# Optimization experiments

Hardware: AMD Instinct MI355X
Metric: run time of the kernel (lower is better)

The kernel has to match this reference:

```python
import jax, jax.numpy as jnp
import numpy as np

A = 9
H = 384
W = 384
MIN_SIZE = 2.0
NMS_THRESH = 0.7
PRE_NMS = 6000
POST_NMS = 300


def _make_anchors():
    # anchors.generate_anchors((H, W), box_sizes): per-cell (x1, y1, w, h) boxes in
    # feature-map coordinates, one box per (anchor, y, x).
    sizes = []
    for s in (4.0, 8.0, 16.0):
        for r in (0.5, 1.0, 2.0):
            sizes.append((s * np.sqrt(r), s / np.sqrt(r)))
    ys, xs = np.meshgrid(np.arange(H, dtype=np.float32), np.arange(W, dtype=np.float32), indexing='ij')
    cx, cy = xs + 0.5, ys + 0.5
    anch = np.stack([
        np.stack([cx - w / 2, cy - h / 2, np.full_like(cx, w), np.full_like(cx, h)], axis=-1)
        for (w, h) in sizes
    ], axis=0)  # [A, H, W, 4]
    return jnp.asarray(anch, jnp.float32)


def setup_inputs() -> dict:
    key = jax.random.key(0)
    k1, k2 = jax.random.split(key)
    scores = jax.random.uniform(k1, (1, A, H, W), dtype=jnp.float32)
    bbox_deltas = jax.random.normal(k2, (1, 4 * A, H, W), dtype=jnp.float32)
    return {
        'scores': scores,
        'bbox_deltas': bbox_deltas,
        'anchor_boxes': _make_anchors(),
        'image_metadata': jnp.zeros((1, 3), jnp.float32),
    }


def _clip_boxes(boxes, length, width):
    # clip_boxes_batch: clamp everything to >=0, convert (x,y,w,h)->(x1,y1,x2,y2),
    # clip to feature-map bounds, convert back.
    b = jnp.maximum(boxes, 0.0)
    x1, y1, w, h = b[..., 0], b[..., 1], b[..., 2], b[..., 3]
    x2 = x1 + w - 1.0
    y2 = y1 + h - 1.0
    x1 = jnp.minimum(x1, length - 1.0)
    y1 = jnp.minimum(y1, width - 1.0)
    x2 = jnp.minimum(x2, length - 1.0)
    y2 = jnp.minimum(y2, width - 1.0)
    return jnp.stack([x1, y1, x2 - x1 + 1.0, y2 - y1 + 1.0], axis=-1)


def _nms(boxes, valid):
    # Faithful port of the source's sequential NMS: repeatedly pick the remaining
    # box with the largest y2, suppress boxes whose intersection / own-area >= thresh.
    x1, y1, w, h = boxes[:, 0], boxes[:, 1], boxes[:, 2], boxes[:, 3]
    x2 = x1 + w - 1.0
    y2 = y1 + h - 1.0
    areas = w * h
    NEG = jnp.float32(-1e30)

    def cond(st):
        v, keep, cnt = st
        return (cnt < POST_NMS) & jnp.any(v)

    def body(st):
        v, keep, cnt = st
        ind = jnp.argmax(jnp.where(v, y2, NEG))
        xx1 = jnp.maximum(x1, x1[ind])
        yy1 = jnp.maximum(y1, y1[ind])
        xx2 = jnp.minimum(x2, x2[ind])
        yy2 = jnp.minimum(y2, y2[ind])
        inter = jnp.maximum(xx2 - xx1 + 1.0, 0.0) * jnp.maximum(yy2 - yy1 + 1.0, 0.0)
        ratio = inter / areas  # intersection over each candidate's own area (as in source)
        nv = v & (ratio < NMS_THRESH)
        nv = nv.at[ind].set(False)
        return nv, keep.at[cnt].set(ind.astype(jnp.int32)), cnt + 1

    keep0 = jnp.full((POST_NMS,), -1, jnp.int32)
    _, keep, cnt = jax.lax.while_loop(cond, body, (valid, keep0, jnp.int32(0)))
    return keep, cnt


def reference(scores, bbox_deltas, anchor_boxes, image_metadata):
    B = 1
    _, _, Hh, Ww = scores.shape
    # two contiguous .view()s compose to a single reshape
    deltas = bbox_deltas.reshape(B, A, Hh, Ww, 4)
    boxes = anchor_boxes[None] + deltas               # [1, A, H, W, 4]
    clipped = _clip_boxes(boxes, float(Hh), float(Ww))
    keep = (clipped[..., 2] >= MIN_SIZE) & (clipped[..., 3] >= MIN_SIZE)

    N = A * Hh * Ww
    boxes_f = clipped.reshape(N, 4)
    scores_f = scores.reshape(N)
    masked = jnp.where(keep.reshape(N), scores_f, jnp.float32(-jnp.inf))

    # descending score sort, PRE_NMS_TOP_N truncation
    order = jnp.argsort(-masked)[:PRE_NMS]
    props = boxes_f[order]                            # [PRE_NMS, 4]
    sc = masked[order]
    valid = jnp.isfinite(sc)

    keep_idx, cnt = _nms(props, valid)
    sel = props[jnp.maximum(keep_idx, 0)]             # [POST_NMS, 4]
    slot_valid = jnp.arange(POST_NMS) < cnt
    out = jnp.where(slot_valid[:, None], sel, 0.0)[None]  # [1, POST_NMS, 4]
    return out
```

## Files before the change

kernel.cpp:

```cpp
#include <hip/hip_runtime.h>
#include <stdint.h>

#define NN 1327104
#define NQ 331776
#define NB 1296
#define PRE_NMS_ 6000
#define POST_NMS_ 300
#define LB_CAP 16384
#define NPAD 6144
#define NWORD 96
#define KB 24
#define MATB 192
#define NREP 8


static __device__ __forceinline__ uint32_t score_key(float s) {
  uint32_t b = __float_as_uint(s);
  uint32_t u = b ^ (((int32_t)b < 0) ? 0xFFFFFFFFu : 0x80000000u);
  return ~u;
}

static __device__ __forceinline__ uint32_t f2s(float v) {
  uint32_t b = __float_as_uint(v);
  return b ^ (((int32_t)b < 0) ? 0xFFFFFFFFu : 0x80000000u);
}

static __device__ __forceinline__ void compute_box(float4 an, float4 de,
    float& x1, float& y1, float& wc, float& hc, bool& keep) {
  float bx = fmaxf(an.x + de.x, 0.0f);
  float by = fmaxf(an.y + de.y, 0.0f);
  float bw = fmaxf(an.z + de.z, 0.0f);
  float bh = fmaxf(an.w + de.w, 0.0f);
  float x2 = bx + bw - 1.0f;
  float y2 = by + bh - 1.0f;
  x1 = fminf(bx, 383.0f);
  y1 = fminf(by, 383.0f);
  x2 = fminf(x2, 383.0f);
  y2 = fminf(y2, 383.0f);
  wc = x2 - x1 + 1.0f;
  hc = y2 - y1 + 1.0f;
  keep = (wc >= 2.0f) && (hc >= 2.0f);
}

static __device__ __forceinline__ uint32_t kb18_of(float s) {
  return (uint32_t)(s * 262144.0f);
}

static __device__ __forceinline__ uint32_t wscan(uint32_t v, int l) {
  #pragma unroll
  for (int off = 1; off < 64; off <<= 1) {
    uint32_t u = __shfl_up(v, off);
    if (l >= off) v += u;
  }
  return v;
}

static __device__ __forceinline__ void pick1_f(const uint32_t* __restrict__ h1r,
                                               uint32_t& selR8, uint32_t& base1) {
  int l = threadIdx.x & 63;
  uint32_t a0 = 0, a1 = 0, a2 = 0, a3 = 0, a4 = 0;
  #pragma unroll
  for (int r = 0; r < NREP; ++r) {
    const uint32_t* h1 = h1r + r * 320;
    a0 += h1[l*5]; a1 += h1[l*5+1]; a2 += h1[l*5+2]; a3 += h1[l*5+3]; a4 += h1[l*5+4];
  }
  uint32_t c0 = a0, c1 = c0+a1, c2 = c1+a2, c3 = c2+a3, c4 = c3+a4;
  uint32_t inc = wscan(c4, l);
  uint32_t excl = inc - c4;
  bool hit = (excl < PRE_NMS_) && (inc >= PRE_NMS_);
  unsigned long long hb = __ballot(hit);
  int hl = __ffsll(hb) - 1;
  uint32_t k, cb;
  if      (excl + c0 >= PRE_NMS_) { k = 0; cb = 0;  }
  else if (excl + c1 >= PRE_NMS_) { k = 1; cb = c0; }
  else if (excl + c2 >= PRE_NMS_) { k = 2; cb = c1; }
  else if (excl + c3 >= PRE_NMS_) { k = 3; cb = c2; }
  else                            { k = 4; cb = c3; }
  selR8 = __shfl(l*5u + k, hl);
  base1 = __shfl(excl + cb, hl);
}

static __device__ __forceinline__ void pickT_lds(const uint32_t* __restrict__ h2,
                                                 uint32_t T,
                                                 uint32_t& sel10, uint32_t& base) {
  int l = threadIdx.x & 63;
  uint32_t h[16];
  #pragma unroll
  for (int k = 0; k < 16; ++k) h[k] = h2[l*16 + k];
  uint32_t cum[16]; cum[0] = h[0];
  #pragma unroll
  for (int k = 1; k < 16; ++k) cum[k] = cum[k-1] + h[k];
  uint32_t inc = wscan(cum[15], l);
  uint32_t excl = inc - cum[15];
  bool hit = (excl < T) && (inc >= T);
  unsigned long long hb = __ballot(hit);
  int hl = __ffsll(hb) - 1;
  uint32_t k = 15, cb = cum[14];
  #pragma unroll
  for (int kk = 15; kk >= 0; --kk)
    if (excl + cum[kk] >= T) { k = (uint32_t)kk; cb = kk ? cum[kk-1] : 0u; }
  sel10 = __shfl(l*16u + k, hl);
  base  = __shfl(excl + cb, hl);
}

static __device__ __forceinline__ void emit_item(uint32_t pos, uint32_t d, uint32_t idx,
    const float4* __restrict__ deltas, const float4* __restrict__ anchors,
    uint64_t* __restrict__ keyhi, uint32_t* __restrict__ keylo,
    float4* __restrict__ box4u) {
  float x1, y1, wc, hc; bool keep;
  compute_box(anchors[idx], deltas[idx], x1, y1, wc, hc, keep);
  float y2 = y1 + hc - 1.0f;
  keyhi[pos] = ((uint64_t)f2s(y2) << 32) | (uint32_t)(~d);
  keylo[pos] = ~idx;
  box4u[pos] = make_float4(x1, y1, wc, hc);
}

__global__ __launch_bounds__(256) void k_hA(const float* __restrict__ scores,
                                            const float4* __restrict__ deltas,
                                            const float4* __restrict__ anchors,
                                            uint32_t* __restrict__ darr,
                                            uint32_t* __restrict__ hist1r,
                                            uint32_t* __restrict__ zctr) {
  __shared__ uint32_t lh[320];
  int t = threadIdx.x;
  for (int j = t; j < 320; j += 256) lh[j] = 0;
  __syncthreads();
  int base = blockIdx.x * 256 + t;
  #pragma unroll
  for (int it = 0; it < 4; ++it) {
    int i = base + it * NQ;
    float x1, y1, wc, hc; bool keep;
    compute_box(anchors[i], deltas[i], x1, y1, wc, hc, keep);
    float s = scores[i];
    uint32_t d = keep ? score_key(s) : 0xFF800000u;
    darr[i] = d;
    uint32_t r8 = keep ? (255u - (kb18_of(s) >> 10)) : 256u;
    atomicAdd(&lh[r8], 1u);
  }
  __syncthreads();
  uint32_t* hdst = hist1r + (blockIdx.x & (NREP - 1)) * 320;
  for (int j = t; j < 320; j += 256) {
    uint32_t c = lh[j];
    if (c) atomicAdd(&hdst[j], c);
  }
  if (blockIdx.x == 0) for (int j = t; j < 320; j += 256) zctr[j] = 0;
}

__global__ __launch_bounds__(256) void k_gather(const uint4* __restrict__ dv,
                                                const uint32_t* __restrict__ hist1r,
                                                uint32_t* __restrict__ ctr,
                                                uint64_t* __restrict__ Lb,
                                                uint64_t* __restrict__ keyhi,
                                                uint32_t* __restrict__ keylo,
                                                float4* __restrict__ box4u,
                                                const float4* __restrict__ deltas,
                                                const float4* __restrict__ anchors) {
  __shared__ uint64_t stA[1024];
  __shared__ uint64_t stB[1024];
  __shared__ uint32_t nA, nB, baseA, baseB, s_sel8;
  int t = threadIdx.x;
  if (t < 64) {
    uint32_t sel8, base1;
    pick1_f(hist1r, sel8, base1);
    if (t == 0) { s_sel8 = sel8; nA = 0; nB = 0; }
  }
  __syncthreads();
  uint32_t selR8 = s_sel8;

  int g = blockIdx.x * 256 + t;
  uint4 v = dv[g];
  uint32_t arr[4] = {v.x, v.y, v.z, v.w};
  #pragma unroll
  for (int k = 0; k < 4; ++k) {
    uint32_t d = arr[k];
    uint32_t idx = (uint32_t)(g * 4 + k);
    uint32_t r8 = (d <= 0x7FFFFFFFu)
                ? (255u - (kb18_of(__uint_as_float(0x7FFFFFFFu - d)) >> 10)) : 256u;
    if (r8 < selR8) {
      uint32_t p = atomicAdd(&nA, 1u);
      stA[p] = ((uint64_t)d << 32) | idx;
    } else if (r8 == selR8) {
      uint32_t q = atomicAdd(&nB, 1u);
      stB[q] = ((uint64_t)d << 32) | idx;
    }
  }
  __syncthreads();
  if (t == 0) {
    baseA = nA ? atomicAdd(&ctr[0], nA)  : 0u;
    baseB = nB ? atomicAdd(&ctr[32], nB) : 0u;
  }
  __syncthreads();
  uint32_t mA = nA, mB = nB, bA = baseA, bB = baseB;
  for (uint32_t j = t; j < mA; j += 256) {
    uint64_t kj = stA[j];
    uint32_t p = bA + j;
    if (p < PRE_NMS_)
      emit_item(p, (uint32_t)(kj >> 32), (uint32_t)kj, deltas, anchors,
                keyhi, keylo, box4u);
  }
  for (uint32_t j = t; j < mB; j += 256) {
    uint32_t q = bB + j;
    if (q < LB_CAP) Lb[q] = stB[j];
  }
}

__global__ __launch_bounds__(256) void k_finish(const uint32_t* __restrict__ ctr,
                                                const uint64_t* __restrict__ Lb,
                                                uint64_t* __restrict__ keyhi,
                                                uint32_t* __restrict__ keylo,
                                                float4* __restrict__ box4u,
                                                const float4* __restrict__ deltas,
                                                const float4* __restrict__ anchors) {
  __shared__ uint32_t lh2[1024];
  __shared__ uint64_t bnd[256];
  __shared__ uint32_t bcnt, lcnt, s_sel10, s_base;
  int t = threadIdx.x;
  for (int j = t; j < 1024; j += 256) lh2[j] = 0;
  if (t == 0) { bcnt = 0; lcnt = 0; }
  __syncthreads();

  uint32_t C1 = ctr[0]; if (C1 > PRE_NMS_) C1 = PRE_NMS_;
  uint32_t Cb = ctr[32]; if (Cb > LB_CAP) Cb = LB_CAP;
  uint32_t T = PRE_NMS_ - C1;

  for (uint32_t j = t; j < Cb; j += 256) {
    uint32_t d = (uint32_t)(Lb[j] >> 32);
    uint32_t r10 = (d <= 0x7FFFFFFFu)
                 ? (1023u - (kb18_of(__uint_as_float(0x7FFFFFFFu - d)) & 1023u)) : 0u;
    atomicAdd(&lh2[r10], 1u);
  }
  __syncthreads();
  if (t < 64) {
    uint32_t sel10 = 0xFFFFFFFFu, b2 = 0;
    if (T > 0) pickT_lds(lh2, T, sel10, b2);
    if (t == 0) { s_sel10 = sel10; s_base = b2; }
  }
  __syncthreads();
  uint32_t sel10 = s_sel10, C2base = s_base;

  for (uint32_t j = t; j < Cb; j += 256) {
    uint64_t kj = Lb[j];
    uint32_t d = (uint32_t)(kj >> 32), idx = (uint32_t)kj;
    uint32_t r10 = (d <= 0x7FFFFFFFu)
                 ? (1023u - (kb18_of(__uint_as_float(0x7FFFFFFFu - d)) & 1023u)) : 0u;
    if (r10 < sel10) {
      uint32_t p = C1 + atomicAdd(&lcnt, 1u);
      if (p < PRE_NMS_) emit_item(p, d, idx, deltas, anchors, keyhi, keylo, box4u);
    } else if (r10 == sel10) {
      uint32_t q = atomicAdd(&bcnt, 1u);
      if (q < 256) bnd[q] = kj;
    }
  }
  __syncthreads();
  uint32_t B = (bcnt < 256u) ? bcnt : 256u;
  uint32_t T2 = (T > C2base) ? (T - C2base) : 0u;
  for (uint32_t j = t; j < B; j += 256) {
    uint64_t kj = bnd[j];
    uint32_t r = 0;
    for (uint32_t k = 0; k < B; ++k) r += (bnd[k] < kj) ? 1u : 0u;
    if (r < T2)
      emit_item(C1 + C2base + r, (uint32_t)(kj >> 32), (uint32_t)kj,
                deltas, anchors, keyhi, keylo, box4u);
  }
  for (int j = PRE_NMS_ + t; j < NPAD; j += 256) {
    keyhi[j] = 0;
    keylo[j] = (uint32_t)(NPAD - j);
    box4u[j] = make_float4(0.f, 0.f, 0.f, 0.f);
  }
}

__global__ __launch_bounds__(512) void k_rank(const uint64_t* __restrict__ keyhi,
                                              const uint32_t* __restrict__ keylo,
                                              uint32_t* __restrict__ rank2d) {
  __shared__ uint64_t shi[768];
  __shared__ uint32_t slo[768];
  int t = threadIdx.x;
  int ib = blockIdx.x >> 3, c = blockIdx.x & 7, base = c * 768;
  for (int j = t; j < 768; j += 512) { shi[j] = keyhi[base + j]; slo[j] = keylo[base + j]; }
  __syncthreads();
  int i = ib * 256 + (t >> 1);
  int h = t & 1;
  uint64_t hi = keyhi[i]; uint32_t lo = keylo[i];
  uint32_t cnt = 0;
  int j0 = h * 384;
  for (int j = j0; j < j0 + 384; ++j) {
    uint64_t hj = shi[j]; uint32_t lj = slo[j];
    cnt += ((hj > hi) || (hj == hi && lj > lo)) ? 1u : 0u;
  }
  rank2d[i * 16 + c * 2 + h] = cnt;
}

__global__ __launch_bounds__(512) void k_matsc(const uint64_t* __restrict__ keyhi,
                                               const uint32_t* __restrict__ rank2d,
                                               const float4* __restrict__ box4u,
                                               float4* __restrict__ sobox,
                                               unsigned long long* __restrict__ valid,
                                               uint64_t* __restrict__ M) {
  __shared__ float4 sb[NPAD];
  __shared__ float  sa[NPAD];
  int t = threadIdx.x;
  int b = blockIdx.x;
  for (int i = t; i < NPAD; i += 512) {
    const uint4* rp = (const uint4*)(rank2d + (size_t)i * 16);
    uint4 r0 = rp[0], r1 = rp[1], r2 = rp[2], r3 = rp[3];
    uint32_t r = r0.x+r0.y+r0.z+r0.w + r1.x+r1.y+r1.z+r1.w
               + r2.x+r2.y+r2.z+r2.w + r3.x+r3.y+r3.z+r3.w;
    float4 bx = box4u[i];
    float x2 = bx.x + bx.z - 1.0f;
    float y2 = bx.y + bx.w - 1.0f;
    sb[r] = make_float4(bx.x, bx.y, x2, y2);
    sa[r] = bx.z * bx.w;
    if (b == 0) {
      sobox[r] = bx;
      uint32_t d = ~(uint32_t)(keyhi[i] & 0xFFFFFFFFu);
      if (d < 0xFF800000u)
        atomicOr(&valid[r >> 6], 1ull << (r & 63));
    }
  }
  __syncthreads();
  int wid = t >> 6, l = t & 63;
  #pragma unroll
  for (int rr = 0; rr < 4; ++rr) {
    int r = b * 32 + wid * 4 + rr;
    float4 rb = sb[r];
    for (int w = 0; w < NWORD; ++w) {
      int j = w * 64 + l;
      float4 cb = sb[j];
      float ca = sa[j];
      float xx1 = fmaxf(cb.x, rb.x), yy1 = fmaxf(cb.y, rb.y);
      float xx2 = fminf(cb.z, rb.z), yy2 = fminf(cb.w, rb.w);
      float iw = fmaxf(xx2 - xx1 + 1.0f, 0.0f);
      float ih = fmaxf(yy2 - yy1 + 1.0f, 0.0f);
      float ratio = (iw * ih) / ca;
      unsigned long long mm = __ballot(!(ratio < 0.7f));
      if (l == 0) M[(size_t)r * NWORD + w] = mm;
    }
  }
}

#define FOR24(F) F(0) F(1) F(2) F(3) F(4) F(5) F(6) F(7) \
                 F(8) F(9) F(10) F(11) F(12) F(13) F(14) F(15) \
                 F(16) F(17) F(18) F(19) F(20) F(21) F(22) F(23)

__global__ __launch_bounds__(512) void k_seq(const unsigned long long* __restrict__ valid,
                                             const uint64_t* __restrict__ M,
                                             const float4* __restrict__ sobox,
                                             float* __restrict__ out) {
  __shared__ int cslot[KB];
  int t = threadIdx.x;
  if (t >= 64) {
    const uint4* p = (const uint4*)M;
    uint4 acc = make_uint4(0, 0, 0, 0);
    for (int j = t - 64; j < 3072 * 48; j += 448) {
      uint4 v = p[j];
      acc.x ^= v.x; acc.y ^= v.y; acc.z ^= v.z; acc.w ^= v.w;
    }
    asm volatile("" :: "v"(acc.x), "v"(acc.y), "v"(acc.z), "v"(acc.w));
    return;
  }
  __builtin_amdgcn_s_setprio(1);
  int l = t;
  unsigned long long v0 = valid[l];
  unsigned long long v1 = (l < 32) ? valid[64 + l] : 0ull;
  uint32_t cnt = 0;

  for (;;) {
    if (cnt >= POST_NMS_) break;
    uint32_t n0 = (uint32_t)__popcll(v0);
    uint32_t inc0 = wscan(n0, l);
    uint32_t T0 = __shfl(inc0, 63);
    uint32_t ex0 = inc0 - n0;
    uint32_t n1 = (uint32_t)__popcll(v1);
    uint32_t inc1 = wscan(n1, l);
    uint32_t T1 = __shfl(inc1, 63);
    uint32_t ex1 = T0 + inc1 - n1;
    uint32_t TV = T0 + T1;
    if (TV == 0) break;
    uint32_t m = (TV < KB) ? TV : KB;

    if (l < KB) cslot[l] = 0;
    __builtin_amdgcn_sched_barrier(0);
    if (ex0 < KB) {
      unsigned long long w = v0; uint32_t r = ex0;
      while (w && r < KB) { int b = __ffsll(w) - 1; cslot[r] = l * 64 + b; ++r; w &= w - 1; }
    }
    if (ex1 < KB && v1) {
      unsigned long long w = v1; uint32_t r = ex1;
      while (w && r < KB) { int b = __ffsll(w) - 1; cslot[r] = (64 + l) * 64 + b; ++r; w &= w - 1; }
    }
    __builtin_amdgcn_sched_barrier(0);

    int cu0 = cslot[0];
#define CUDECL(k) int cu_##k = cslot[k];
    FOR24(CUDECL)
#undef CUDECL
    int c_own = (l < KB) ? cslot[l] : cu0;
    uint32_t ow = (uint32_t)c_own >> 6, ob = (uint32_t)c_own & 63;

#define ROWDECL(k) uint64_t rm0_##k = 0, rm1_##k = 0;
    FOR24(ROWDECL)
#undef ROWDECL
#define ROWLOAD(k) if (k < (int)m) { const uint64_t* rp = M + (size_t)cu_##k * NWORD; \
                     rm0_##k = rp[l]; rm1_##k = (l < 32) ? rp[64 + l] : 0ull; }
    FOR24(ROWLOAD)
#undef ROWLOAD
    uint32_t col = 0;
#define COLLOAD(k) if (k < (int)m) { \
                     uint64_t wq = M[(size_t)cu_##k * NWORD + ow]; \
                     col |= (uint32_t)((wq >> ob) & 1ull) << k; }
    FOR24(COLLOAD)
#undef COLLOAD
    float4 obox = make_float4(0.f, 0.f, 0.f, 0.f);
    if (l < KB) obox = sobox[c_own];

    uint32_t cnt0 = cnt;
    uint32_t wm = 0;
#define GREEDY(k) { \
      unsigned long long bal = __ballot((l == k) && ((col & wm) == 0u)); \
      if ((k < (int)m) && (cnt < POST_NMS_) && ((bal >> k) & 1ull)) { \
        wm |= 1u << k; ++cnt; } }
    FOR24(GREEDY)
#undef GREEDY

    if (l < KB && ((wm >> l) & 1)) {
      uint32_t pos = cnt0 + (uint32_t)__popc(wm & ((1u << l) - 1));
      *(float4*)(out + (size_t)pos * 4) = obox;
    }

    uint64_t comb0 = 0, comb1 = 0;
#define COMB(k) if ((wm >> k) & 1) { comb0 |= rm0_##k; comb1 |= rm1_##k; }
    FOR24(COMB)
#undef COMB
    v0 &= ~comb0; v1 &= ~comb1;
  }
  __builtin_amdgcn_s_setprio(0);

  for (int j = l; j < (int)(POST_NMS_ - cnt) * 4; j += 64) out[cnt * 4 + j] = 0.0f;
}

extern "C" void kernel_launch(void* const* d_in, const int* in_sizes, int n_in,
                              void* d_out, int out_size, void* d_ws, size_t ws_size,
                              hipStream_t stream) {
  const float*  scores  = (const float*)d_in[0];
  const float4* deltas  = (const float4*)d_in[1];
  const float4* anchors = (const float4*)d_in[2];
  float* out = (float*)d_out;

  uint8_t* w8 = (uint8_t*)d_ws;
  uint32_t* darr  = (uint32_t*)w8;
  uint64_t* M     = (uint64_t*)w8;
  float4*   sobox = (float4*)(w8 + 4841472);
  uint64_t* keyhi  = (uint64_t*)(w8 + 5308416);
  uint32_t* keylo  = (uint32_t*)(w8 + 5357568);
  float4*   box4u  = (float4*)  (w8 + 5382144);
  uint32_t* rank2d = (uint32_t*)(w8 + 5480448);
  uint32_t* hist1r = (uint32_t*)(w8 + 5873664);
  uint32_t* ctr    = (uint32_t*)(w8 + 5883904);
  unsigned long long* valid = (unsigned long long*)(w8 + 5884160);
  uint64_t* Lb     = (uint64_t*)(w8 + 5885184);

  const uint4* dv = (const uint4*)darr;

  hipMemsetAsync(hist1r, 0, 10240, stream);

  k_hA    <<<NB, 256, 0, stream>>>(scores, deltas, anchors, darr, hist1r, ctr);
  k_gather<<<NB, 256, 0, stream>>>(dv, hist1r, ctr, Lb, keyhi, keylo, box4u,
                                   deltas, anchors);
  k_finish<<<1, 256, 0, stream>>>(ctr, Lb, keyhi, keylo, box4u, deltas, anchors);
  k_rank  <<<MATB, 512, 0, stream>>>(keyhi, keylo, rank2d);
  k_matsc <<<MATB, 512, 0, stream>>>(keyhi, rank2d, box4u, sobox, valid, M);
  k_seq   <<<1, 512, 0, stream>>>(valid, M, sobox, out);
}
```

Baseline: 304.7 us.

## Replace precomputed IoU bitmask matrix with on-the-fly block NMS in one workgroup

Drops the 6144x6144 suppression-matrix kernel and the bitmask-driven sequential pass. NMS now runs in a single 1024-thread workgroup. Each round takes the next 64 valid candidates, resolves them greedily against each other with a wavefront-local IoU row, then all threads suppress the remaining candidates against the newly kept boxes. This removes the large matrix build and its global-memory traffic. In exchange the whole NMS runs on one CU with per-round barriers and data-dependent loops over the kept list. The zctr clear range also shrinks to 64 entries.

```diff
diff --git a/kernel.cpp b/kernel.cpp
--- a/kernel.cpp
+++ b/kernel.cpp
@@ -9,7 +9,6 @@
 #define LB_CAP 16384
 #define NPAD 6144
 #define NWORD 96
-#define KB 24
 #define MATB 192
 #define NREP 8
 
@@ -143,7 +142,7 @@
     uint32_t c = lh[j];
     if (c) atomicAdd(&hdst[j], c);
   }
-  if (blockIdx.x == 0) for (int j = t; j < 320; j += 256) zctr[j] = 0;
+  if (blockIdx.x == 0) for (int j = t; j < 64; j += 256) zctr[j] = 0;
 }
 
 __global__ __launch_bounds__(256) void k_gather(const uint4* __restrict__ dv,
@@ -290,152 +289,129 @@
   rank2d[i * 16 + c * 2 + h] = cnt;
 }
 
-__global__ __launch_bounds__(512) void k_matsc(const uint64_t* __restrict__ keyhi,
-                                               const uint32_t* __restrict__ rank2d,
-                                               const float4* __restrict__ box4u,
-                                               float4* __restrict__ sobox,
-                                               unsigned long long* __restrict__ valid,
-                                               uint64_t* __restrict__ M) {
-  __shared__ float4 sb[NPAD];
-  __shared__ float  sa[NPAD];
+__global__ __launch_bounds__(1024) void k_seq(const uint32_t* __restrict__ rank2d,
+                                              const float4* __restrict__ box4u,
+                                              const uint64_t* __restrict__ keyhi,
+                                              float* __restrict__ out) {
+  __shared__ float4 sob[NPAD];
+  __shared__ unsigned long long vw[NWORD];
+  __shared__ int cslot[64];
+  __shared__ int wlist[64];
+  __shared__ uint32_t s_nw, s_cnt, s_done;
   int t = threadIdx.x;
-  int b = blockIdx.x;
-  for (int i = t; i < NPAD; i += 512) {
+  if (t < NWORD) vw[t] = 0ull;
+  if (t == 0) { s_cnt = 0; s_done = 0; s_nw = 0; }
+  __syncthreads();
+  for (int i = t; i < NPAD; i += 1024) {
     const uint4* rp = (const uint4*)(rank2d + (size_t)i * 16);
     uint4 r0 = rp[0], r1 = rp[1], r2 = rp[2], r3 = rp[3];
     uint32_t r = r0.x+r0.y+r0.z+r0.w + r1.x+r1.y+r1.z+r1.w
                + r2.x+r2.y+r2.z+r2.w + r3.x+r3.y+r3.z+r3.w;
     float4 bx = box4u[i];
-    float x2 = bx.x + bx.z - 1.0f;
-    float y2 = bx.y + bx.w - 1.0f;
-    sb[r] = make_float4(bx.x, bx.y, x2, y2);
-    sa[r] = bx.z * bx.w;
-    if (b == 0) {
-      sobox[r] = bx;
-      uint32_t d = ~(uint32_t)(keyhi[i] & 0xFFFFFFFFu);
-      if (d < 0xFF800000u)
-        atomicOr(&valid[r >> 6], 1ull << (r & 63));
+    sob[r] = bx;
+    uint32_t d = ~(uint32_t)(keyhi[i] & 0xFFFFFFFFu);
+    if (d < 0xFF800000u)
+      atomicOr(&vw[r >> 6], 1ull << (r & 63));
+  }
+  __syncthreads();
+
+  int wid = t >> 6, l = t & 63;
+  for (;;) {
+    if (wid == 0) {
+      unsigned long long v0 = vw[l];
+      unsigned long long v1 = (l < 32) ? vw[64 + l] : 0ull;
+      uint32_t n0 = (uint32_t)__popcll(v0);
+      uint32_t inc0 = wscan(n0, l);
+      uint32_t T0 = __shfl(inc0, 63);
+      uint32_t ex0 = inc0 - n0;
+      uint32_t n1 = (uint32_t)__popcll(v1);
+      uint32_t inc1 = wscan(n1, l);
+      uint32_t T1 = __shfl(inc1, 63);
+      uint32_t ex1 = T0 + inc1 - n1;
+      uint32_t TV = T0 + T1;
+      uint32_t m = (TV < 64u) ? TV : 64u;
+      cslot[l] = 0;
+      __builtin_amdgcn_sched_barrier(0);
+      if (ex0 < 64 && v0) {
+        unsigned long long w = v0; uint32_t r = ex0;
+        while (w && r < 64) { int b = __ffsll(w) - 1; cslot[r] = l * 64 + b; ++r; w &= w - 1; }
+      }
+      if (ex1 < 64 && v1) {
+        unsigned long long w = v1; uint32_t r = ex1;
+        while (w && r < 64) { int b = __ffsll(w) - 1; cslot[r] = (64 + l) * 64 + b; ++r; w &= w - 1; }
+      }
+      __builtin_amdgcn_sched_barrier(0);
+
+      uint32_t cnt = s_cnt;
+      uint32_t done = 0, nw = 0;
+      if (m == 0 || cnt >= POST_NMS_) {
+        done = 1;
+      } else {
+        int cown = cslot[(l < (int)m) ? l : 0];
+        float4 bq = sob[cown];
+        float x1k = bq.x, y1k = bq.y;
+        float x2k = bq.x + bq.z - 1.0f, y2k = bq.y + bq.w - 1.0f;
+        unsigned long long row = 0;
+        for (uint32_t j = 0; j < m; ++j) {
+          float4 bj = sob[cslot[j]];
+          float x1j = bj.x, y1j = bj.y;
+          float x2j = bj.x + bj.z - 1.0f, y2j = bj.y + bj.w - 1.0f;
+          float area = bj.z * bj.w;
+          float xx1 = fmaxf(x1j, x1k), yy1 = fmaxf(y1j, y1k);
+          float xx2 = fminf(x2j, x2k), yy2 = fminf(y2j, y2k);
+          float iw = fmaxf(xx2 - xx1 + 1.0f, 0.0f);
+          float ih = fmaxf(yy2 - yy1 + 1.0f, 0.0f);
+          float ratio = (iw * ih) / area;
+          if (!(ratio < 0.7f)) row |= 1ull << j;
+        }
+        unsigned long long supp = 0, wm = 0;
+        uint32_t cnt0 = cnt;
+        for (uint32_t k = 0; k < m && cnt < POST_NMS_; ++k) {
+          if (!((supp >> k) & 1ull)) {
+            wm |= 1ull << k; ++cnt;
+            unsigned long long rowk = __shfl(row, (int)k);
+            supp |= rowk;
+          }
+        }
+        nw = cnt - cnt0;
+        if (l < (int)m && ((wm >> l) & 1ull)) {
+          uint32_t pos = cnt0 + (uint32_t)__popcll(wm & ((1ull << l) - 1ull));
+          *(float4*)(out + (size_t)pos * 4) = bq;
+          wlist[pos - cnt0] = cown;
+        }
+        if (cnt >= POST_NMS_) done = 1;
+      }
+      if (l == 0) { s_cnt = cnt; s_nw = nw; s_done = done; }
     }
-  }
-  __syncthreads();
-  int wid = t >> 6, l = t & 63;
-  #pragma unroll
-  for (int rr = 0; rr < 4; ++rr) {
-    int r = b * 32 + wid * 4 + rr;
-    float4 rb = sb[r];
-    for (int w = 0; w < NWORD; ++w) {
-      int j = w * 64 + l;
-      float4 cb = sb[j];
-      float ca = sa[j];
-      float xx1 = fmaxf(cb.x, rb.x), yy1 = fmaxf(cb.y, rb.y);
-      float xx2 = fminf(cb.z, rb.z), yy2 = fminf(cb.w, rb.w);
-      float iw = fmaxf(xx2 - xx1 + 1.0f, 0.0f);
-      float ih = fmaxf(yy2 - yy1 + 1.0f, 0.0f);
-      float ratio = (iw * ih) / ca;
-      unsigned long long mm = __ballot(!(ratio < 0.7f));
-      if (l == 0) M[(size_t)r * NWORD + w] = mm;
+    __syncthreads();
+    if (s_done) break;
+    uint32_t nw = s_nw;
+    #pragma unroll
+    for (int it = 0; it < NPAD / 1024; ++it) {
+      int j = t + it * 1024;
+      unsigned long long wv = vw[j >> 6];
+      if (!((wv >> (j & 63)) & 1ull)) continue;
+      float4 bj = sob[j];
+      float x1j = bj.x, y1j = bj.y;
+      float x2j = bj.x + bj.z - 1.0f, y2j = bj.y + bj.w - 1.0f;
+      float area = bj.z * bj.w;
+      bool kill = false;
+      for (uint32_t w2 = 0; w2 < nw && !kill; ++w2) {
+        float4 bw = sob[wlist[w2]];
+        float x2w = bw.x + bw.z - 1.0f, y2w = bw.y + bw.w - 1.0f;
+        float xx1 = fmaxf(x1j, bw.x), yy1 = fmaxf(y1j, bw.y);
+        float xx2 = fminf(x2j, x2w), yy2 = fminf(y2j, y2w);
+        float iw = fmaxf(xx2 - xx1 + 1.0f, 0.0f);
+        float ih = fmaxf(yy2 - yy1 + 1.0f, 0.0f);
+        float ratio = (iw * ih) / area;
+        if (!(ratio < 0.7f)) kill = true;
+      }
+      if (kill) atomicAnd(&vw[j >> 6], ~(1ull << (j & 63)));
     }
-  }
-}
-
-#define FOR24(F) F(0) F(1) F(2) F(3) F(4) F(5) F(6) F(7) \
-                 F(8) F(9) F(10) F(11) F(12) F(13) F(14) F(15) \
-                 F(16) F(17) F(18) F(19) F(20) F(21) F(22) F(23)
-
-__global__ __launch_bounds__(512) void k_seq(const unsigned long long* __restrict__ valid,
-                                             const uint64_t* __restrict__ M,
-                                             const float4* __restrict__ sobox,
-                                             float* __restrict__ out) {
-  __shared__ int cslot[KB];
-  int t = threadIdx.x;
-  if (t >= 64) {
-    const uint4* p = (const uint4*)M;
-    uint4 acc = make_uint4(0, 0, 0, 0);
-    for (int j = t - 64; j < 3072 * 48; j += 448) {
-      uint4 v = p[j];
-      acc.x ^= v.x; acc.y ^= v.y; acc.z ^= v.z; acc.w ^= v.w;
-    }
-    asm volatile("" :: "v"(acc.x), "v"(acc.y), "v"(acc.z), "v"(acc.w));
-    return;
-  }
-  __builtin_amdgcn_s_setprio(1);
-  int l = t;
-  unsigned long long v0 = valid[l];
-  unsigned long long v1 = (l < 32) ? valid[64 + l] : 0ull;
-  uint32_t cnt = 0;
-
-  for (;;) {
-    if (cnt >= POST_NMS_) break;
-    uint32_t n0 = (uint32_t)__popcll(v0);
-    uint32_t inc0 = wscan(n0, l);
-    uint32_t T0 = __shfl(inc0, 63);
-    uint32_t ex0 = inc0 - n0;
-    uint32_t n1 = (uint32_t)__popcll(v1);
-    uint32_t inc1 = wscan(n1, l);
-    uint32_t T1 = __shfl(inc1, 63);
-    uint32_t ex1 = T0 + inc1 - n1;
-    uint32_t TV = T0 + T1;
-    if (TV == 0) break;
-    uint32_t m = (TV < KB) ? TV : KB;
-
-    if (l < KB) cslot[l] = 0;
-    __builtin_amdgcn_sched_barrier(0);
-    if (ex0 < KB) {
-      unsigned long long w = v0; uint32_t r = ex0;
-      while (w && r < KB) { int b = __ffsll(w) - 1; cslot[r] = l * 64 + b; ++r; w &= w - 1; }
-    }
-    if (ex1 < KB && v1) {
-      unsigned long long w = v1; uint32_t r = ex1;
-      while (w && r < KB) { int b = __ffsll(w) - 1; cslot[r] = (64 + l) * 64 + b; ++r; w &= w - 1; }
-    }
-    __builtin_amdgcn_sched_barrier(0);
-
-    int cu0 = cslot[0];
-#define CUDECL(k) int cu_##k = cslot[k];
-    FOR24(CUDECL)
-#undef CUDECL
-    int c_own = (l < KB) ? cslot[l] : cu0;
-    uint32_t ow = (uint32_t)c_own >> 6, ob = (uint32_t)c_own & 63;
-
-#define ROWDECL(k) uint64_t rm0_##k = 0, rm1_##k = 0;
-    FOR24(ROWDECL)
-#undef ROWDECL
-#define ROWLOAD(k) if (k < (int)m) { const uint64_t* rp = M + (size_t)cu_##k * NWORD; \
-                     rm0_##k = rp[l]; rm1_##k = (l < 32) ? rp[64 + l] : 0ull; }
-    FOR24(ROWLOAD)
-#undef ROWLOAD
-    uint32_t col = 0;
-#define COLLOAD(k) if (k < (int)m) { \
-                     uint64_t wq = M[(size_t)cu_##k * NWORD + ow]; \
-                     col |= (uint32_t)((wq >> ob) & 1ull) << k; }
-    FOR24(COLLOAD)
-#undef COLLOAD
-    float4 obox = make_float4(0.f, 0.f, 0.f, 0.f);
-    if (l < KB) obox = sobox[c_own];
-
-    uint32_t cnt0 = cnt;
-    uint32_t wm = 0;
-#define GREEDY(k) { \
-      unsigned long long bal = __ballot((l == k) && ((col & wm) == 0u)); \
-      if ((k < (int)m) && (cnt < POST_NMS_) && ((bal >> k) & 1ull)) { \
-        wm |= 1u << k; ++cnt; } }
-    FOR24(GREEDY)
-#undef GREEDY
-
-    if (l < KB && ((wm >> l) & 1)) {
-      uint32_t pos = cnt0 + (uint32_t)__popc(wm & ((1u << l) - 1));
-      *(float4*)(out + (size_t)pos * 4) = obox;
-    }
-
-    uint64_t comb0 = 0, comb1 = 0;
-#define COMB(k) if ((wm >> k) & 1) { comb0 |= rm0_##k; comb1 |= rm1_##k; }
-    FOR24(COMB)
-#undef COMB
-    v0 &= ~comb0; v1 &= ~comb1;
-  }
-  __builtin_amdgcn_s_setprio(0);
-
-  for (int j = l; j < (int)(POST_NMS_ - cnt) * 4; j += 64) out[cnt * 4 + j] = 0.0f;
+    __syncthreads();
+  }
+  uint32_t cnt = s_cnt;
+  for (int j = t; j < (int)(POST_NMS_ - cnt) * 4; j += 1024) out[cnt * 4 + j] = 0.0f;
 }
 
 extern "C" void kernel_launch(void* const* d_in, const int* in_sizes, int n_in,
@@ -448,15 +424,12 @@
 
   uint8_t* w8 = (uint8_t*)d_ws;
   uint32_t* darr  = (uint32_t*)w8;
-  uint64_t* M     = (uint64_t*)w8;
-  float4*   sobox = (float4*)(w8 + 4841472);
   uint64_t* keyhi  = (uint64_t*)(w8 + 5308416);
   uint32_t* keylo  = (uint32_t*)(w8 + 5357568);
   float4*   box4u  = (float4*)  (w8 + 5382144);
   uint32_t* rank2d = (uint32_t*)(w8 + 5480448);
   uint32_t* hist1r = (uint32_t*)(w8 + 5873664);
   uint32_t* ctr    = (uint32_t*)(w8 + 5883904);
-  unsigned long long* valid = (unsigned long long*)(w8 + 5884160);
   uint64_t* Lb     = (uint64_t*)(w8 + 5885184);
 
   const uint4* dv = (const uint4*)darr;
@@ -468,6 +441,5 @@
                                    deltas, anchors);
   k_finish<<<1, 256, 0, stream>>>(ctr, Lb, keyhi, keylo, box4u, deltas, anchors);
   k_rank  <<<MATB, 512, 0, stream>>>(keyhi, keylo, rank2d);
-  k_matsc <<<MATB, 512, 0, stream>>>(keyhi, rank2d, box4u, sobox, valid, M);
-  k_seq   <<<1, 512, 0, stream>>>(valid, M, sobox, out);
-}
+  k_seq   <<<1, 1024, 0, stream>>>(rank2d, box4u, keyhi, out);
+}
```

Measured after the change: 550.8 us. +80.8%, slower.

## Shrink sequential NMS batch to 16 and drop cache-prefetch helper waves

Applied to the files above, without the earlier changes.

The single-block greedy NMS kernel now runs as one 64-lane wavefront instead of 512 threads. The extra waves that streamed the mask matrix to warm the cache, and the priority boost, are removed. The candidate batch per iteration drops from 24 to 16, which cuts the row and column loads and the serial ballot steps per round. The second valid-word scan is skipped when the first 64 words already hold enough candidates. The trade-off is more loop iterations per kept box, and mask-row loads that may miss in cache without the warm-up waves.

```diff
diff --git a/kernel.cpp b/kernel.cpp
--- a/kernel.cpp
+++ b/kernel.cpp
@@ -9,7 +9,7 @@
 #define LB_CAP 16384
 #define NPAD 6144
 #define NWORD 96
-#define KB 24
+#define KB 16
 #define MATB 192
 #define NREP 8
 
@@ -338,28 +338,15 @@
   }
 }
 
-#define FOR24(F) F(0) F(1) F(2) F(3) F(4) F(5) F(6) F(7) \
-                 F(8) F(9) F(10) F(11) F(12) F(13) F(14) F(15) \
-                 F(16) F(17) F(18) F(19) F(20) F(21) F(22) F(23)
-
-__global__ __launch_bounds__(512) void k_seq(const unsigned long long* __restrict__ valid,
-                                             const uint64_t* __restrict__ M,
-                                             const float4* __restrict__ sobox,
-                                             float* __restrict__ out) {
+#define FOR16(F) F(0) F(1) F(2) F(3) F(4) F(5) F(6) F(7) \
+                 F(8) F(9) F(10) F(11) F(12) F(13) F(14) F(15)
+
+__global__ __launch_bounds__(64) void k_seq(const unsigned long long* __restrict__ valid,
+                                            const uint64_t* __restrict__ M,
+                                            const float4* __restrict__ sobox,
+                                            float* __restrict__ out) {
   __shared__ int cslot[KB];
-  int t = threadIdx.x;
-  if (t >= 64) {
-    const uint4* p = (const uint4*)M;
-    uint4 acc = make_uint4(0, 0, 0, 0);
-    for (int j = t - 64; j < 3072 * 48; j += 448) {
-      uint4 v = p[j];
-      acc.x ^= v.x; acc.y ^= v.y; acc.z ^= v.z; acc.w ^= v.w;
-    }
-    asm volatile("" :: "v"(acc.x), "v"(acc.y), "v"(acc.z), "v"(acc.w));
-    return;
-  }
-  __builtin_amdgcn_s_setprio(1);
-  int l = t;
+  int l = threadIdx.x;
   unsigned long long v0 = valid[l];
   unsigned long long v1 = (l < 32) ? valid[64 + l] : 0ull;
   uint32_t cnt = 0;
@@ -370,13 +357,18 @@
     uint32_t inc0 = wscan(n0, l);
     uint32_t T0 = __shfl(inc0, 63);
     uint32_t ex0 = inc0 - n0;
-    uint32_t n1 = (uint32_t)__popcll(v1);
-    uint32_t inc1 = wscan(n1, l);
-    uint32_t T1 = __shfl(inc1, 63);
-    uint32_t ex1 = T0 + inc1 - n1;
-    uint32_t TV = T0 + T1;
-    if (TV == 0) break;
-    uint32_t m = (TV < KB) ? TV : KB;
+    uint32_t m, ex1 = KB;
+    if (T0 < KB) {
+      uint32_t n1 = (uint32_t)__popcll(v1);
+      uint32_t inc1 = wscan(n1, l);
+      uint32_t T1 = __shfl(inc1, 63);
+      uint32_t TV = T0 + T1;
+      if (TV == 0) break;
+      m = (TV < KB) ? TV : KB;
+      ex1 = T0 + inc1 - n1;
+    } else {
+      m = KB;
+    }
 
     if (l < KB) cslot[l] = 0;
     __builtin_amdgcn_sched_barrier(0);
@@ -390,25 +382,24 @@
     }
     __builtin_amdgcn_sched_barrier(0);
 
-    int cu0 = cslot[0];
 #define CUDECL(k) int cu_##k = cslot[k];
-    FOR24(CUDECL)
+    FOR16(CUDECL)
 #undef CUDECL
-    int c_own = (l < KB) ? cslot[l] : cu0;
+    int c_own = cslot[(l < KB) ? l : 0];
     uint32_t ow = (uint32_t)c_own >> 6, ob = (uint32_t)c_own & 63;
 
 #define ROWDECL(k) uint64_t rm0_##k = 0, rm1_##k = 0;
-    FOR24(ROWDECL)
+    FOR16(ROWDECL)
 #undef ROWDECL
-#define ROWLOAD(k) if (k < (int)m) { const uint64_t* rp = M + (size_t)cu_##k * NWORD; \
-                     rm0_##k = rp[l]; rm1_##k = (l < 32) ? rp[64 + l] : 0ull; }
-    FOR24(ROWLOAD)
+#define ROWLOAD(k) if (k < (int)m) { const uint64_t* p = M + (size_t)cu_##k * NWORD; \
+                     rm0_##k = p[l]; rm1_##k = (l < 32) ? p[64 + l] : 0ull; }
+    FOR16(ROWLOAD)
 #undef ROWLOAD
     uint32_t col = 0;
 #define COLLOAD(k) if (k < (int)m) { \
                      uint64_t wq = M[(size_t)cu_##k * NWORD + ow]; \
                      col |= (uint32_t)((wq >> ob) & 1ull) << k; }
-    FOR24(COLLOAD)
+    FOR16(COLLOAD)
 #undef COLLOAD
     float4 obox = make_float4(0.f, 0.f, 0.f, 0.f);
     if (l < KB) obox = sobox[c_own];
@@ -419,7 +410,7 @@
       unsigned long long bal = __ballot((l == k) && ((col & wm) == 0u)); \
       if ((k < (int)m) && (cnt < POST_NMS_) && ((bal >> k) & 1ull)) { \
         wm |= 1u << k; ++cnt; } }
-    FOR24(GREEDY)
+    FOR16(GREEDY)
 #undef GREEDY
 
     if (l < KB && ((wm >> l) & 1)) {
@@ -429,11 +420,10 @@
 
     uint64_t comb0 = 0, comb1 = 0;
 #define COMB(k) if ((wm >> k) & 1) { comb0 |= rm0_##k; comb1 |= rm1_##k; }
-    FOR24(COMB)
+    FOR16(COMB)
 #undef COMB
     v0 &= ~comb0; v1 &= ~comb1;
   }
-  __builtin_amdgcn_s_setprio(0);
 
   for (int j = l; j < (int)(POST_NMS_ - cnt) * 4; j += 64) out[cnt * 4 + j] = 0.0f;
 }
@@ -469,5 +459,5 @@
   k_finish<<<1, 256, 0, stream>>>(ctr, Lb, keyhi, keylo, box4u, deltas, anchors);
   k_rank  <<<MATB, 512, 0, stream>>>(keyhi, keylo, rank2d);
   k_matsc <<<MATB, 512, 0, stream>>>(keyhi, rank2d, box4u, sobox, valid, M);
-  k_seq   <<<1, 512, 0, stream>>>(valid, M, sobox, out);
-}
+  k_seq   <<<1, 64, 0, stream>>>(valid, M, sobox, out);
+}
```

Result: faster. 273.0 us (-10.4%).
